# Kernel optimization log

Hardware: AMD Instinct MI355X
Metric: run time of the kernel (lower is better)

## Reference

```python
import jax, jax.numpy as jnp
import numpy as np

N = 1024      # number of nodes
D = 128       # d_x
H = 8         # num_heads


def setup_inputs() -> dict:
    key = jax.random.key(0)
    ks = jax.random.split(key, 7)
    s = (D * H) ** -0.5
    return {
        "x": jax.random.normal(ks[0], (N, D), dtype=jnp.float32),
        "spatial_encoding": jax.random.normal(ks[1], (N, N), dtype=jnp.float32),
        "edge_encoding": jax.random.normal(ks[2], (N, N), dtype=jnp.float32),
        "Wq": jax.random.normal(ks[3], (D * H, D), dtype=jnp.float32) * s,
        "Wk": jax.random.normal(ks[4], (D * H, D), dtype=jnp.float32) * s,
        "Wv": jax.random.normal(ks[5], (D * H, D), dtype=jnp.float32) * s,
        "Wo": jax.random.normal(ks[6], (D, D * H), dtype=jnp.float32) * s,
    }


def reference(x, spatial_encoding, edge_encoding, Wq, Wk, Wv, Wo):
    n, d = x.shape
    h = Wq.shape[0] // d
    scale = d ** -0.5
    # Linear (no bias), then the module's peculiar view: [n, d*h] -> [d, n, h]
    q = (x @ Wq.T).reshape(d, n, h)            # [d, n, h]
    k = (x @ Wk.T).reshape(d, n, h)            # [d, n, h]
    v = (x @ Wv.T).reshape(d, n, h)            # [d, n, h]
    # a = q @ k^T over head dim: [d, n, n]
    a = jnp.einsum('dnh,dmh->dnm', q, k) * scale
    a = a + spatial_encoding + edge_encoding   # [n,n] biases broadcast over d
    a = jax.nn.softmax(a, axis=2)
    # dropout is identity at inference
    out = jnp.einsum('dnm,dmh->dnh', a, v)     # [d, n, h]
    out = out.reshape(n, h * d)                # row-major reshape, same as torch
    return out @ Wo.T                          # [n, d]
```

## Files before the change

### kernel.cpp

```cpp
#include <hip/hip_runtime.h>
#include <hip/hip_bf16.h>
#include <math.h>

#define N_NODES 1024
#define D_DIM   128
#define H_HEADS 8
#define DH      1024

typedef short  short8 __attribute__((ext_vector_type(8)));
typedef float  f32x16 __attribute__((ext_vector_type(16)));
typedef float  f32x4  __attribute__((ext_vector_type(4)));

static __device__ __forceinline__ unsigned short f2bf(float x) {
    __hip_bfloat16 h = __float2bfloat16(x);
    return *reinterpret_cast<unsigned short*>(&h);
}
static __device__ __forceinline__ unsigned cvt_pk_bf16(float lo, float hi) {
    unsigned r;
    asm volatile("v_cvt_pk_bf16_f32 %0, %1, %2" : "=v"(r) : "v"(lo), "v"(hi));
    return r;
}
static __device__ __forceinline__ void permlane32_swap(unsigned &a, unsigned &b) {
    asm volatile("v_permlane32_swap_b32 %0, %1" : "+v"(a), "+v"(b));
}
static __device__ __forceinline__ float fast_exp2(float x) {
    float r;
    asm("v_exp_f32 %0, %1" : "=v"(r) : "v"(x));
    return r;
}

__global__ __launch_bounds__(256) void prep_kernel(
        const float* __restrict__ x,  const float* __restrict__ Wq,
        const float* __restrict__ Wk, const float* __restrict__ Wv,
        const float* __restrict__ sp, const float* __restrict__ ed,
        const float* __restrict__ Wo,
        unsigned short* __restrict__ Qb, unsigned short* __restrict__ Kb,
        unsigned short* __restrict__ Vb, float* __restrict__ Bq,
        unsigned short* __restrict__ Woh, unsigned short* __restrict__ Wol) {
    __shared__ float tile[32][33];
    const int u   = blockIdx.x;
    const int tid = threadIdx.x;

    if (u < 768) {
        const int lane = tid & 63, wvi = tid >> 6;
        const int l31 = lane & 31, hi = lane >> 5;
        const int m   = u >> 8;
        const int rem = u & 255;
        const int rb0 = (rem & 7) * 128 + wvi * 32;
        const int col = (rem >> 3) * 32 + l31;
        const float* W        = (m == 0) ? Wq : (m == 1) ? Wk : Wv;
        unsigned short* Out   = (m == 0) ? Qb : (m == 1) ? Kb : Vb;
        const float osc = (m == 0) ? 0.12751879523173864f : 1.0f;

        const float* xrow = x + (size_t)(rb0 + l31) * 128 + 8 * hi;
        const float* wrow = W + (size_t)col * 128 + 8 * hi;

        f32x16 acc = {};
        #pragma unroll
        for (int ks = 0; ks < 8; ++ks) {
            float4 xa = *reinterpret_cast<const float4*>(xrow + ks * 16);
            float4 xb = *reinterpret_cast<const float4*>(xrow + ks * 16 + 4);
            float4 wa = *reinterpret_cast<const float4*>(wrow + ks * 16);
            float4 wb = *reinterpret_cast<const float4*>(wrow + ks * 16 + 4);
            union { short8 s8; unsigned uu[4]; } af, bf;
            af.uu[0] = cvt_pk_bf16(xa.x, xa.y); af.uu[1] = cvt_pk_bf16(xa.z, xa.w);
            af.uu[2] = cvt_pk_bf16(xb.x, xb.y); af.uu[3] = cvt_pk_bf16(xb.z, xb.w);
            bf.uu[0] = cvt_pk_bf16(wa.x, wa.y); bf.uu[1] = cvt_pk_bf16(wa.z, wa.w);
            bf.uu[2] = cvt_pk_bf16(wb.x, wb.y); bf.uu[3] = cvt_pk_bf16(wb.z, wb.w);
            acc = __builtin_amdgcn_mfma_f32_32x32x16_bf16(af.s8, bf.s8, acc, 0, 0, 0);
        }
        #pragma unroll
        for (int i = 0; i < 16; ++i) {
            int mm = (i & 3) + 8 * (i >> 2) + 4 * hi;
            Out[(size_t)(rb0 + mm) * DH + col] = f2bf(acc[i] * osc);
        }
    } else if (u < 1792) {
        const int b2 = u - 768;
        const int cb = b2 & 31, rb = b2 >> 5;
        const float L2E = 1.4426950408889634f;
        for (int i = tid; i < 1024; i += 256) {
            int rr = i >> 5, cc = i & 31;
            size_t g = (size_t)(rb * 32 + rr) * 1024 + cb * 32 + cc;
            tile[rr][cc] = (sp[g] + ed[g]) * L2E;
        }
        __syncthreads();
        const int c4l = tid >> 5, rr = tid & 31;
        float4 v = make_float4(tile[rr][4 * c4l + 0], tile[rr][4 * c4l + 1],
                               tile[rr][4 * c4l + 2], tile[rr][4 * c4l + 3]);
        reinterpret_cast<float4*>(Bq)[(size_t)(cb * 8 + c4l) * 1024 + rb * 32 + rr] = v;
    } else {
        const int b2 = u - 1792;
        const size_t base = (size_t)b2 * 4096 + (size_t)tid * 16;
        #pragma unroll
        for (int t = 0; t < 4; ++t) {
            float4 w = *reinterpret_cast<const float4*>(Wo + base + t * 4);
            float ww[4] = { w.x, w.y, w.z, w.w };
            unsigned short h4[4], l4[4];
            #pragma unroll
            for (int j = 0; j < 4; ++j) {
                unsigned uv = __float_as_uint(ww[j]);
                h4[j] = (unsigned short)(uv >> 16);
                l4[j] = f2bf(ww[j] - __uint_as_float(uv & 0xFFFF0000u));
            }
            *reinterpret_cast<uint2*>(Woh + base + t * 4) = *reinterpret_cast<uint2*>(h4);
            *reinterpret_cast<uint2*>(Wol + base + t * 4) = *reinterpret_cast<uint2*>(l4);
        }
    }
}

static __device__ __forceinline__ void stage_vt(const unsigned short* __restrict__ src,
                                                char* base, int tid) {
    #pragma unroll
    for (int it = 0; it < 2; ++it) {
        int pr = it * 256 + tid;
        short8 v0 = *reinterpret_cast<const short8*>(src + (size_t)(2 * pr) * 8);
        short8 v1 = *reinterpret_cast<const short8*>(src + (size_t)(2 * pr + 1) * 8);
        #pragma unroll
        for (int h = 0; h < 8; ++h) {
            unsigned d = (unsigned)(unsigned short)v0[h] |
                         ((unsigned)(unsigned short)v1[h] << 16);
            *reinterpret_cast<unsigned*>(base + h * 2048 + ((4 * pr) ^ (h << 4))) = d;
        }
    }
    reinterpret_cast<unsigned*>(base + 16384)[tid]       = 0x3F803F80u;
    reinterpret_cast<unsigned*>(base + 16384)[tid + 256] = 0x3F803F80u;
}

static __device__ __forceinline__ f32x16 load_bias16(const float4* bq4, int cbv) {
    const float4* b = bq4 + (size_t)cbv * 8192;
    float4 b0 = b[0], b1 = b[2048], b2 = b[4096], b3 = b[6144];
    f32x16 o;
    o[0]  = b0.x; o[1]  = b0.y; o[2]  = b0.z; o[3]  = b0.w;
    o[4]  = b1.x; o[5]  = b1.y; o[6]  = b1.z; o[7]  = b1.w;
    o[8]  = b2.x; o[9]  = b2.y; o[10] = b2.z; o[11] = b2.w;
    o[12] = b3.x; o[13] = b3.y; o[14] = b3.z; o[15] = b3.w;
    return o;
}

static __device__ __forceinline__ void attn_step(int cbv, const f32x16& bias,
                                                 const short8& kfv, const short8& qfv,
                                                 const char* vbs, int vswz, int hi,
                                                 f32x16& oacc) {
    f32x16 sf = bias;
    sf = __builtin_amdgcn_mfma_f32_32x32x16_bf16(kfv, qfv, sf, 0, 0, 0);
    float p[16];
    #pragma unroll
    for (int i = 0; i < 16; ++i) p[i] = fast_exp2(sf[i]);
    unsigned u0 = cvt_pk_bf16(p[0],  p[1]);
    unsigned u1 = cvt_pk_bf16(p[2],  p[3]);
    unsigned u2 = cvt_pk_bf16(p[4],  p[5]);
    unsigned u3 = cvt_pk_bf16(p[6],  p[7]);
    unsigned u4 = cvt_pk_bf16(p[8],  p[9]);
    unsigned u5 = cvt_pk_bf16(p[10], p[11]);
    unsigned u6 = cvt_pk_bf16(p[12], p[13]);
    unsigned u7 = cvt_pk_bf16(p[14], p[15]);
    permlane32_swap(u0, u2);
    permlane32_swap(u1, u3);
    permlane32_swap(u4, u6);
    permlane32_swap(u5, u7);
    union { short8 s8; unsigned uu[4]; } pb1, pb2;
    pb1.uu[0] = u0; pb1.uu[1] = u1; pb1.uu[2] = u2; pb1.uu[3] = u3;
    pb2.uu[0] = u4; pb2.uu[1] = u5; pb2.uu[2] = u6; pb2.uu[3] = u7;

    short8 vf1 = *reinterpret_cast<const short8*>(vbs + ((cbv * 64 + 16 * hi)      ^ vswz));
    short8 vf2 = *reinterpret_cast<const short8*>(vbs + ((cbv * 64 + 32 + 16 * hi) ^ vswz));
    oacc = __builtin_amdgcn_mfma_f32_32x32x16_bf16(vf1, pb1.s8, oacc, 0, 0, 0);
    oacc = __builtin_amdgcn_mfma_f32_32x32x16_bf16(vf2, pb2.s8, oacc, 0, 0, 0);
}

static __device__ __forceinline__ void attn_epilogue(const f32x16& oa, int dd, int r, int hi,
                                                     unsigned short* __restrict__ Oh,
                                                     unsigned short* __restrict__ Ol) {
    const float ls = oa[4];
    const float rl = 1.f / ls;
    unsigned short h4[4], l4[4];
    #pragma unroll
    for (int i = 0; i < 4; ++i) {
        float v = oa[i] * rl;
        unsigned uv = __float_as_uint(v);
        h4[i] = (unsigned short)(uv >> 16);
        l4[i] = f2bf(v - __uint_as_float(uv & 0xFFFF0000u));
    }
    size_t off = (size_t)dd * 8192 + (size_t)r * 8 + 4 * hi;
    *reinterpret_cast<uint2*>(Oh + off) = *reinterpret_cast<uint2*>(h4);
    *reinterpret_cast<uint2*>(Ol + off) = *reinterpret_cast<uint2*>(l4);
}

__global__ __launch_bounds__(256) void attn2_kernel(
        const unsigned short* __restrict__ Qb, const unsigned short* __restrict__ Kb,
        const unsigned short* __restrict__ Vb, const float* __restrict__ Bq,
        unsigned short* __restrict__ Oh, unsigned short* __restrict__ Ol) {
    __shared__ __align__(16) char smraw[36864];
    const int un = blockIdx.x, tid = threadIdx.x;
    const int rbx = un & 7, dp = un >> 3;
    const int lane = tid & 63, wvi = tid >> 6;
    const int l31 = lane & 31, hi = lane >> 5;

    stage_vt(Vb + (size_t)(2 * dp) * 8192,     smraw,         tid);
    stage_vt(Vb + (size_t)(2 * dp + 1) * 8192, smraw + 18432, tid);
    __syncthreads();

    const int r = rbx * 128 + wvi * 32 + l31;
    short8 qf0 = {}, qf1 = {};
    if (!hi) {
        qf0 = *reinterpret_cast<const short8*>(Qb + (size_t)(2 * dp)     * 8192 + (size_t)r * 8);
        qf1 = *reinterpret_cast<const short8*>(Qb + (size_t)(2 * dp + 1) * 8192 + (size_t)r * 8);
    }
    f32x16 o0 = {}, o1 = {};
    const unsigned short* kp0 = Kb + (size_t)(2 * dp) * 8192 + (size_t)l31 * 8;
    const unsigned short* kp1 = kp0 + 8192;
    const float4* bq4 = reinterpret_cast<const float4*>(Bq) + (size_t)hi * 1024 + r;
    const int vrow = (l31 < 8) ? l31 : 8;
    const char* vb0 = smraw + vrow * 2048;
    const char* vb1 = smraw + 18432 + vrow * 2048;
    const int vswz = vrow << 4;

    f32x16 bA = load_bias16(bq4, 0), bB = load_bias16(bq4, 1);
    short8 kA0 = *reinterpret_cast<const short8*>(kp0);
    short8 kA1 = *reinterpret_cast<const short8*>(kp1);
    short8 kB0 = *reinterpret_cast<const short8*>(kp0 + 256);
    short8 kB1 = *reinterpret_cast<const short8*>(kp1 + 256);
    for (int cb = 0; cb < 32; cb += 2) {
        attn_step(cb, bA, kA0, qf0, vb0, vswz, hi, o0);
        attn_step(cb, bA, kA1, qf1, vb1, vswz, hi, o1);
        if (cb < 30) {
            bA = load_bias16(bq4, cb + 2);
            kA0 = *reinterpret_cast<const short8*>(kp0 + (size_t)(cb + 2) * 256);
            kA1 = *reinterpret_cast<const short8*>(kp1 + (size_t)(cb + 2) * 256);
        }
        attn_step(cb + 1, bB, kB0, qf0, vb0, vswz, hi, o0);
        attn_step(cb + 1, bB, kB1, qf1, vb1, vswz, hi, o1);
        if (cb < 30) {
            bB = load_bias16(bq4, cb + 3);
            kB0 = *reinterpret_cast<const short8*>(kp0 + (size_t)(cb + 3) * 256);
            kB1 = *reinterpret_cast<const short8*>(kp1 + (size_t)(cb + 3) * 256);
        }
    }
    attn_epilogue(o0, 2 * dp,     r, hi, Oh, Ol);
    attn_epilogue(o1, 2 * dp + 1, r, hi, Oh, Ol);
}

__global__ __launch_bounds__(256) void oproj_kernel(
        const unsigned short* __restrict__ Oh, const unsigned short* __restrict__ Ol,
        const unsigned short* __restrict__ Woh, const unsigned short* __restrict__ Wol,
        float* __restrict__ out) {
    __shared__ float red[4][256];
    const int u = blockIdx.x, tid = threadIdx.x;
    const int lane = tid & 63, wvi = tid >> 6;
    const int l15 = lane & 15, kg = lane >> 4;
    const int rbase = (u & 63) * 16, cbase = (u >> 6) * 16;

    const unsigned short* ah_p = Oh  + (size_t)(rbase + l15) * 1024 + wvi * 256 + kg * 8;
    const unsigned short* al_p = Ol  + (size_t)(rbase + l15) * 1024 + wvi * 256 + kg * 8;
    const unsigned short* bh_p = Woh + (size_t)(cbase + l15) * 1024 + wvi * 256 + kg * 8;
    const unsigned short* bl_p = Wol + (size_t)(cbase + l15) * 1024 + wvi * 256 + kg * 8;

    f32x4 acc = {};
    #pragma unroll
    for (int ks = 0; ks < 8; ++ks) {
        short8 ah = *reinterpret_cast<const short8*>(ah_p + ks * 32);
        short8 al = *reinterpret_cast<const short8*>(al_p + ks * 32);
        short8 bh = *reinterpret_cast<const short8*>(bh_p + ks * 32);
        short8 bl = *reinterpret_cast<const short8*>(bl_p + ks * 32);
        acc = __builtin_amdgcn_mfma_f32_16x16x32_bf16(ah, bh, acc, 0, 0, 0);
        acc = __builtin_amdgcn_mfma_f32_16x16x32_bf16(al, bh, acc, 0, 0, 0);
        acc = __builtin_amdgcn_mfma_f32_16x16x32_bf16(ah, bl, acc, 0, 0, 0);
    }
    #pragma unroll
    for (int i = 0; i < 4; ++i)
        red[wvi][(kg * 4 + i) * 16 + l15] = acc[i];
    __syncthreads();
    float v = red[0][tid & 255] + red[1][tid & 255] + red[2][tid & 255] + red[3][tid & 255];
    out[(size_t)(rbase + (tid >> 4)) * D_DIM + cbase + (tid & 15)] = v;
}

extern "C" void kernel_launch(void* const* d_in, const int* in_sizes, int n_in,
                              void* d_out, int out_size, void* d_ws, size_t ws_size,
                              hipStream_t stream) {
    const float* x  = (const float*)d_in[0];
    const float* sp = (const float*)d_in[1];
    const float* ed = (const float*)d_in[2];
    const float* Wq = (const float*)d_in[3];
    const float* Wk = (const float*)d_in[4];
    const float* Wv = (const float*)d_in[5];
    const float* Wo = (const float*)d_in[6];
    float* out = (float*)d_out;

    float* ws = (float*)d_ws;
    const size_t M = (size_t)N_NODES * DH;
    float* Bq = ws;
    unsigned short* Qb = (unsigned short*)(ws + M);
    unsigned short* Kb = Qb + M;
    unsigned short* Vb = Kb + M;
    unsigned short* Oh = Vb + M;
    unsigned short* Ol = Oh + M;
    unsigned short* Woh = Ol + M;
    unsigned short* Wol = Woh + 131072;

    prep_kernel<<<dim3(1824), 256, 0, stream>>>(x, Wq, Wk, Wv, sp, ed, Wo,
                                                Qb, Kb, Vb, Bq, Woh, Wol);
    attn2_kernel<<<dim3(512), 256, 0, stream>>>(Qb, Kb, Vb, Bq, Oh, Ol);
    oproj_kernel<<<dim3(512), 256, 0, stream>>>(Oh, Ol, Woh, Wol, out);
}
```

Before: 61.18 us.

## Make bias layout contiguous per lane and interleave two-head attention steps

The packed bias buffer is re-laid out so each lane's 16 bias values for a column block sit in four consecutive float4s, replacing four loads strided far apart with one contiguous 64-byte read. The attention inner step is also restructured to issue both heads' QK MFMAs, exponentials and PV MFMAs interleaved, giving the scheduler independent work to hide MFMA latency. The producer kernel's write pattern changes to match, which may reduce coalescing of those bias stores. Register pressure rises slightly from holding both heads' intermediates at once.

Result: slower. 62.80 us (+2.6%).

```diff
diff --git a/kernel.cpp b/kernel.cpp
--- a/kernel.cpp
+++ b/kernel.cpp
@@ -84,10 +84,12 @@
             tile[rr][cc] = (sp[g] + ed[g]) * L2E;
         }
         __syncthreads();
-        const int c4l = tid >> 5, rr = tid & 31;
-        float4 v = make_float4(tile[rr][4 * c4l + 0], tile[rr][4 * c4l + 1],
-                               tile[rr][4 * c4l + 2], tile[rr][4 * c4l + 3]);
-        reinterpret_cast<float4*>(Bq)[(size_t)(cb * 8 + c4l) * 1024 + rb * 32 + rr] = v;
+        const int rr  = tid >> 3, rem = tid & 7;
+        const int hi  = rem >> 2, g = rem & 3;
+        const int c0  = 8 * g + 4 * hi;
+        float4 v = make_float4(tile[rr][c0], tile[rr][c0 + 1],
+                               tile[rr][c0 + 2], tile[rr][c0 + 3]);
+        reinterpret_cast<float4*>(Bq)[((size_t)(cb * 2 + hi) * 1024 + rb * 32 + rr) * 4 + g] = v;
     } else {
         const int b2 = u - 1792;
         const size_t base = (size_t)b2 * 4096 + (size_t)tid * 16;
@@ -126,9 +128,8 @@
     reinterpret_cast<unsigned*>(base + 16384)[tid + 256] = 0x3F803F80u;
 }
 
-static __device__ __forceinline__ f32x16 load_bias16(const float4* bq4, int cbv) {
-    const float4* b = bq4 + (size_t)cbv * 8192;
-    float4 b0 = b[0], b1 = b[2048], b2 = b[4096], b3 = b[6144];
+static __device__ __forceinline__ f32x16 load_bias16(const float4* b) {
+    float4 b0 = b[0], b1 = b[1], b2 = b[2], b3 = b[3];
     f32x16 o;
     o[0]  = b0.x; o[1]  = b0.y; o[2]  = b0.z; o[3]  = b0.w;
     o[4]  = b1.x; o[5]  = b1.y; o[6]  = b1.z; o[7]  = b1.w;
@@ -137,15 +138,7 @@
     return o;
 }
 
-static __device__ __forceinline__ void attn_step(int cbv, const f32x16& bias,
-                                                 const short8& kfv, const short8& qfv,
-                                                 const char* vbs, int vswz, int hi,
-                                                 f32x16& oacc) {
-    f32x16 sf = bias;
-    sf = __builtin_amdgcn_mfma_f32_32x32x16_bf16(kfv, qfv, sf, 0, 0, 0);
-    float p[16];
-    #pragma unroll
-    for (int i = 0; i < 16; ++i) p[i] = fast_exp2(sf[i]);
+static __device__ __forceinline__ void pack_p(const float* p, short8& pb1, short8& pb2) {
     unsigned u0 = cvt_pk_bf16(p[0],  p[1]);
     unsigned u1 = cvt_pk_bf16(p[2],  p[3]);
     unsigned u2 = cvt_pk_bf16(p[4],  p[5]);
@@ -158,14 +151,10 @@
     permlane32_swap(u1, u3);
     permlane32_swap(u4, u6);
     permlane32_swap(u5, u7);
-    union { short8 s8; unsigned uu[4]; } pb1, pb2;
-    pb1.uu[0] = u0; pb1.uu[1] = u1; pb1.uu[2] = u2; pb1.uu[3] = u3;
-    pb2.uu[0] = u4; pb2.uu[1] = u5; pb2.uu[2] = u6; pb2.uu[3] = u7;
-
-    short8 vf1 = *reinterpret_cast<const short8*>(vbs + ((cbv * 64 + 16 * hi)      ^ vswz));
-    short8 vf2 = *reinterpret_cast<const short8*>(vbs + ((cbv * 64 + 32 + 16 * hi) ^ vswz));
-    oacc = __builtin_amdgcn_mfma_f32_32x32x16_bf16(vf1, pb1.s8, oacc, 0, 0, 0);
-    oacc = __builtin_amdgcn_mfma_f32_32x32x16_bf16(vf2, pb2.s8, oacc, 0, 0, 0);
+    union { short8 s8; unsigned uu[4]; } a, b;
+    a.uu[0] = u0; a.uu[1] = u1; a.uu[2] = u2; a.uu[3] = u3;
+    b.uu[0] = u4; b.uu[1] = u5; b.uu[2] = u6; b.uu[3] = u7;
+    pb1 = a.s8; pb2 = b.s8;
 }
 
 static __device__ __forceinline__ void attn_epilogue(const f32x16& oa, int dd, int r, int hi,
@@ -209,29 +198,46 @@
     f32x16 o0 = {}, o1 = {};
     const unsigned short* kp0 = Kb + (size_t)(2 * dp) * 8192 + (size_t)l31 * 8;
     const unsigned short* kp1 = kp0 + 8192;
-    const float4* bq4 = reinterpret_cast<const float4*>(Bq) + (size_t)hi * 1024 + r;
+    const float4* bp = reinterpret_cast<const float4*>(Bq) + ((size_t)hi * 1024 + r) * 4;
     const int vrow = (l31 < 8) ? l31 : 8;
     const char* vb0 = smraw + vrow * 2048;
     const char* vb1 = smraw + 18432 + vrow * 2048;
     const int vswz = vrow << 4;
 
-    f32x16 bA = load_bias16(bq4, 0), bB = load_bias16(bq4, 1);
+    auto step2 = [&](int cbv, const f32x16& bias, const short8& k0, const short8& k1) {
+        f32x16 s0 = __builtin_amdgcn_mfma_f32_32x32x16_bf16(k0, qf0, bias, 0, 0, 0);
+        f32x16 s1 = __builtin_amdgcn_mfma_f32_32x32x16_bf16(k1, qf1, bias, 0, 0, 0);
+        float p0[16], p1[16];
+        #pragma unroll
+        for (int i = 0; i < 16; ++i) { p0[i] = fast_exp2(s0[i]); p1[i] = fast_exp2(s1[i]); }
+        short8 pa1, pa2, pb1, pb2;
+        pack_p(p0, pa1, pa2);
+        pack_p(p1, pb1, pb2);
+        short8 va1 = *reinterpret_cast<const short8*>(vb0 + ((cbv * 64 + 16 * hi)      ^ vswz));
+        short8 va2 = *reinterpret_cast<const short8*>(vb0 + ((cbv * 64 + 32 + 16 * hi) ^ vswz));
+        short8 vc1 = *reinterpret_cast<const short8*>(vb1 + ((cbv * 64 + 16 * hi)      ^ vswz));
+        short8 vc2 = *reinterpret_cast<const short8*>(vb1 + ((cbv * 64 + 32 + 16 * hi) ^ vswz));
+        o0 = __builtin_amdgcn_mfma_f32_32x32x16_bf16(va1, pa1, o0, 0, 0, 0);
+        o1 = __builtin_amdgcn_mfma_f32_32x32x16_bf16(vc1, pb1, o1, 0, 0, 0);
+        o0 = __builtin_amdgcn_mfma_f32_32x32x16_bf16(va2, pa2, o0, 0, 0, 0);
+        o1 = __builtin_amdgcn_mfma_f32_32x32x16_bf16(vc2, pb2, o1, 0, 0, 0);
+    };
+
+    f32x16 bA = load_bias16(bp), bB = load_bias16(bp + 8192);
     short8 kA0 = *reinterpret_cast<const short8*>(kp0);
     short8 kA1 = *reinterpret_cast<const short8*>(kp1);
     short8 kB0 = *reinterpret_cast<const short8*>(kp0 + 256);
     short8 kB1 = *reinterpret_cast<const short8*>(kp1 + 256);
     for (int cb = 0; cb < 32; cb += 2) {
-        attn_step(cb, bA, kA0, qf0, vb0, vswz, hi, o0);
-        attn_step(cb, bA, kA1, qf1, vb1, vswz, hi, o1);
+        step2(cb, bA, kA0, kA1);
         if (cb < 30) {
-            bA = load_bias16(bq4, cb + 2);
+            bA  = load_bias16(bp + (size_t)(cb + 2) * 8192);
             kA0 = *reinterpret_cast<const short8*>(kp0 + (size_t)(cb + 2) * 256);
             kA1 = *reinterpret_cast<const short8*>(kp1 + (size_t)(cb + 2) * 256);
         }
-        attn_step(cb + 1, bB, kB0, qf0, vb0, vswz, hi, o0);
-        attn_step(cb + 1, bB, kB1, qf1, vb1, vswz, hi, o1);
+        step2(cb + 1, bB, kB0, kB1);
         if (cb < 30) {
-            bB = load_bias16(bq4, cb + 3);
+            bB  = load_bias16(bp + (size_t)(cb + 3) * 8192);
             kB0 = *reinterpret_cast<const short8*>(kp0 + (size_t)(cb + 3) * 256);
             kB1 = *reinterpret_cast<const short8*>(kp1 + (size_t)(cb + 3) * 256);
         }
```
